# Performance work log

Hardware: AMD Instinct MI355X
Metric: run time of the kernel (lower is better)

## Reference

```python
import jax, jax.numpy as jnp
import numpy as np

B, CIN, H, W = 2, 55, 768, 768
NR, NC = 24, 24      # number of grid-cell rows / cols
CTOP = 36            # block_conv1x1_output[block_num-1] for block_num=2


def _dil_conv_relu(x, w, b, dil):
    # Conv2d(k=5, dilation=dil, padding=2*dil) -> same spatial size, then ReLU
    pad = 2 * dil
    y = jax.lax.conv_general_dilated(
        x, w, window_strides=(1, 1), padding=[(pad, pad), (pad, pad)],
        rhs_dilation=(dil, dil), dimension_numbers=('NCHW', 'OIHW', 'NCHW'))
    return jax.nn.relu(y + b[None, :, None, None])


def setup_inputs() -> dict:
    key = jax.random.key(0)
    ks = jax.random.split(key, 12)
    def p(k, shape, fan_in):
        bound = 1.0 / np.sqrt(fan_in)
        return jax.random.uniform(k, shape, jnp.float32, -bound, bound)
    return {
        'x': jax.random.normal(ks[0], (B, CIN, H, W), dtype=jnp.float32),
        'row_ids': jnp.sort(jax.random.randint(ks[1], (H,), 0, NR)).astype(jnp.int32),
        'col_ids': jnp.sort(jax.random.randint(ks[2], (W,), 0, NC)).astype(jnp.int32),
        'num_row_segs': NR,
        'num_col_segs': NC,
        'w1': p(ks[3], (6, CIN, 5, 5), CIN * 25), 'b1': p(ks[4], (6,), CIN * 25),
        'w2': p(ks[5], (6, CIN, 5, 5), CIN * 25), 'b2': p(ks[6], (6,), CIN * 25),
        'w3': p(ks[7], (6, CIN, 5, 5), CIN * 25), 'b3': p(ks[8], (6,), CIN * 25),
        'w_top': p(ks[9], (CTOP, 18), 18), 'b_top': p(ks[9], (CTOP,), 18),
        'w_bot': p(ks[10], (1, 18), 18), 'b_bot': p(ks[11], (1,), 18),
    }


def reference(x, row_ids, col_ids, num_row_segs, num_col_segs,
              w1, b1, w2, b2, w3, b3, w_top, b_top, w_bot, b_bot):
    b = x.shape[0]
    # --- three dilated conv branches, concat on channels ---
    x1 = _dil_conv_relu(x, w1, b1, 1)
    x2 = _dil_conv_relu(x, w2, b2, 2)
    x3 = _dil_conv_relu(x, w3, b3, 3)
    out_feature = jnp.concatenate((x1, x2, x3), axis=1)  # [B,18,H,W]

    # 1x1 convs as channel matmuls
    top = jnp.einsum('oi,bihw->bohw', w_top, out_feature) + b_top[None, :, None, None]
    bot = jnp.einsum('oi,bihw->bohw', w_bot, out_feature) + b_bot[None, :, None, None]

    # segment one-hot selectors: R [NR,H], C [NC,W]
    R = (row_ids[None, :] == jnp.arange(num_row_segs, dtype=row_ids.dtype)[:, None]).astype(x.dtype)
    C = (col_ids[None, :] == jnp.arange(num_col_segs, dtype=col_ids.dtype)[:, None]).astype(x.dtype)
    cnt = jnp.maximum(R.sum(1)[:, None] * C.sum(1)[None, :], 1.0)  # [NR,NC] cell sizes

    # --- top branch: per-(batch,channel) grid-cell mean, broadcast back ---
    top_sums = jnp.einsum('rh,bkhw,cw->bkrc', R, top, C)           # [B,CTOP,NR,NC]
    top_means = top_sums / cnt
    top_out = top_means[:, :, row_ids, :][:, :, :, col_ids]        # [B,CTOP,H,W]

    # --- bottom branch: mean of sigmoid over cell AND batch (torch.mean over all dims) ---
    sig = jax.nn.sigmoid(bot)                                      # [B,1,H,W]
    bot_sums = jnp.einsum('rh,bkhw,cw->rc', R, sig, C)             # [NR,NC]
    pools_val = bot_sums / (b * cnt)
    bottom_out = jnp.broadcast_to(pools_val[row_ids, :][:, col_ids][None, None],
                                  (b, 1, top.shape[2], top.shape[3]))
    pools = jnp.broadcast_to(pools_val[None, None], (b, 1, num_row_segs, num_col_segs))

    out_x = jnp.concatenate((top_out, out_feature, bottom_out), axis=1)  # [B,55,H,W]
    return out_x, pools
```

## Files before the change

### kernel.cpp

```cpp
#include <hip/hip_runtime.h>
#include <math.h>

#define HH 768
#define WW 768
#define NPIX (HH*WW)
#define NRR 24
#define NCC 24
#define NCELL (NRR*NCC)
#define CTOPC 36
#define NB 2

typedef _Float16 f16x8 __attribute__((ext_vector_type(8)));
typedef float f32x4 __attribute__((ext_vector_type(4)));

__device__ __forceinline__ size_t xt_off(int b) {
  return b ? (size_t)54 * NPIX : 0;
}

#define OFF_WB     0
#define OFF_ZP     38400
#define OFF_FSUM   38656
#define OFF_BOTP   59392
#define OFF_TMEAN  60544
#define OFF_PVAL   102016
#define OFF_BOUNDS 102592

__global__ void prep_kernel(const float* __restrict__ w1, const float* __restrict__ w2,
                            const float* __restrict__ w3,
                            const int* __restrict__ row_ids, const int* __restrict__ col_ids,
                            unsigned int* __restrict__ wB, unsigned int* __restrict__ zp,
                            int* __restrict__ bounds) {
  int t = blockIdx.x * 256 + threadIdx.x;
  if (t < 150 * 256) {
    int frag = t >> 8, r = t & 255;
    int lane = r >> 2, part = r & 3;
    int chb = frag & 1, q = frag >> 1;
    int d = q / 25, tap = q % 25;
    int ky = tap / 5, kx = tap % 5;
    int oc = lane & 15;
    int kk = (lane >> 4) * 8 + part * 2;
    int ch0 = chb * 32 + kk, ch1 = ch0 + 1;
    const float* ws_ = (d == 0) ? w1 : ((d == 1) ? w2 : w3);
    float f0 = (oc < 6 && ch0 < 55) ? ws_[((oc * 55 + ch0) * 5 + ky) * 5 + kx] : 0.f;
    float f1 = (oc < 6 && ch1 < 55) ? ws_[((oc * 55 + ch1) * 5 + ky) * 5 + kx] : 0.f;
    _Float16 g0 = (_Float16)f0, g1 = (_Float16)f1;
    wB[t] = (unsigned int)__builtin_bit_cast(unsigned short, g0) |
            ((unsigned int)__builtin_bit_cast(unsigned short, g1) << 16);
  }
  if (blockIdx.x == 1 && threadIdx.x < 256) zp[threadIdx.x] = 0u;
  if (blockIdx.x == 0 && threadIdx.x < 48) {
    int tt = threadIdx.x;
    const int* ids = (tt < 24) ? row_ids : col_ids;
    int r = tt % 24;
    int s = HH, e = HH;
    for (int h = 0; h < HH; ++h) {
      int v = ids[h];
      if (v >= r && h < s) s = h;
      if (v >= r + 1 && h < e) e = h;
    }
    int base = (tt < 24) ? 0 : 48;
    bounds[base + r] = s;
    bounds[base + 24 + r] = e;
  }
}

__global__ __launch_bounds__(256) void xpose_kernel(const float* __restrict__ x,
                                                    unsigned int* __restrict__ outU) {
  const int b = blockIdx.y;
  const int px = blockIdx.x * 256 + threadIdx.x;
  const float* xb = x + (size_t)b * 55 * NPIX + px;
  unsigned int buf[32];
  #pragma unroll
  for (int cp = 0; cp < 27; ++cp) {
    float f0 = xb[(size_t)(2 * cp) * NPIX];
    float f1 = xb[(size_t)(2 * cp + 1) * NPIX];
    buf[cp] = __builtin_bit_cast(unsigned int, __builtin_amdgcn_cvt_pkrtz(f0, f1));
  }
  buf[27] = __builtin_bit_cast(unsigned int, __builtin_amdgcn_cvt_pkrtz(xb[(size_t)54 * NPIX], 0.f));
  buf[28] = buf[29] = buf[30] = buf[31] = 0u;
  unsigned int* dst = outU + xt_off(b) + (size_t)px * 32;
  #pragma unroll
  for (int i = 0; i < 8; ++i) ((uint4*)dst)[i] = *(uint4*)&buf[i * 4];
}

__global__ __attribute__((amdgpu_flat_work_group_size(384, 384)))
           __attribute__((amdgpu_waves_per_eu(2, 3)))
void conv_kernel(const unsigned int* __restrict__ outU_c,
                 const unsigned int* __restrict__ wB,
                 const unsigned int* __restrict__ zp,
                 const float* __restrict__ b1, const float* __restrict__ b2,
                 const float* __restrict__ b3, float* __restrict__ out) {
  __shared__ __align__(16) unsigned int tile[17600];
  const int tid = threadIdx.x;
  const int lane = tid & 63, wave = tid >> 6;
  const int d = wave >> 1, hh = wave & 1, dil = d + 1;
  const int b = blockIdx.z;
  const int h0 = blockIdx.y * 8, w0 = blockIdx.x * 32;
  const unsigned int* xTb = outU_c + xt_off(b);
  const int col = lane & 15, kq = lane >> 4;

  f32x4 acc[8];
  #pragma unroll
  for (int u = 0; u < 8; ++u) acc[u] = (f32x4){0.f, 0.f, 0.f, 0.f};

  for (int chb = 0; chb < 2; ++chb) {
    #pragma unroll
    for (int k = 0; k < 10; ++k) {
      int idx = k * 384 + tid;
      if (idx < 3520) {
        int pxl = idx >> 2, part = idx & 3;
        int th = pxl / 44, tw = pxl % 44;
        int gh = h0 - 6 + th, gw = w0 - 6 + tw;
        bool ok = ((unsigned)gh < 768u) & ((unsigned)gw < 768u);
        const unsigned int* src = ok
            ? xTb + ((size_t)(gh * 768 + gw)) * 32 + chb * 16 + part * 4
            : zp + (tid & 63) * 4;
        uint4 v = *(const uint4*)src;
        *(uint4*)&tile[pxl * 20 + part * 4] = v;
      }
    }
    __syncthreads();
    for (int ky = 0; ky < 5; ++ky) {
      #pragma unroll
      for (int kx = 0; kx < 5; ++kx) {
        const int fidx = ((d * 25 + ky * 5 + kx) * 2 + chb) << 8;
        f16x8 bfrag = __builtin_bit_cast(f16x8, *(const uint4*)(wB + fidx + lane * 4));
        const int dy = (ky - 2) * dil, dx = (kx - 2) * dil;
        const int thb = hh * 4 + 6 + dy;
        const int twb = col + 6 + dx;
        #pragma unroll
        for (int u = 0; u < 8; ++u) {
          int hr = u >> 1, pc = u & 1;
          int a_addr = ((thb + hr) * 44 + twb + pc * 16) * 20 + kq * 4;
          f16x8 afrag = __builtin_bit_cast(f16x8, *(const uint4*)&tile[a_addr]);
          acc[u] = __builtin_amdgcn_mfma_f32_16x16x32_f16(afrag, bfrag, acc[u], 0, 0, 0);
        }
      }
    }
    __syncthreads();
  }

  float* ot = (float*)tile;
  if (col < 6) {
    #pragma unroll
    for (int u = 0; u < 8; ++u) {
      int hr = hh * 4 + (u >> 1), pc = u & 1;
      int oc = d * 6 + col;
      #pragma unroll
      for (int reg = 0; reg < 4; ++reg) {
        int px = kq * 4 + reg;
        ot[(oc * 8 + hr) * 32 + pc * 16 + px] = acc[u][reg];
      }
    }
  }
  __syncthreads();
  #pragma unroll
  for (int k = 0; k < 3; ++k) {
    int i = k * 384 + tid;
    int oc = i >> 6, rem = i & 63;
    int hr = rem >> 3, f4 = rem & 7;
    float bias = oc < 6 ? b1[oc] : (oc < 12 ? b2[oc - 6] : b3[oc - 12]);
    float4 v = ((float4*)ot)[i];
    v.x = fmaxf(v.x + bias, 0.f); v.y = fmaxf(v.y + bias, 0.f);
    v.z = fmaxf(v.z + bias, 0.f); v.w = fmaxf(v.w + bias, 0.f);
    *(float4*)(out + ((size_t)(b * 55 + 36 + oc)) * NPIX
               + (size_t)(h0 + hr) * 768 + w0 + f4 * 4) = v;
  }
}

__global__ __launch_bounds__(256) void cellsum_kernel(const float* __restrict__ dout,
    const int* __restrict__ bounds,
    const float* __restrict__ w_bot, const float* __restrict__ b_bot,
    float* __restrict__ feat_sums, float* __restrict__ bot_partial) {
  int blk = blockIdx.x;
  int b = blk / NCELL; int rc = blk % NCELL; int r = rc / NCC, c = rc % NCC;
  int rs = bounds[r], re = bounds[24 + r], cs = bounds[48 + c], ce = bounds[72 + c];
  int cw = ce - cs;
  int npix = (re - rs) * cw;
  float facc[18];
  #pragma unroll
  for (int k = 0; k < 18; ++k) facc[k] = 0.f;
  float sacc = 0.f;
  float wb[18];
  #pragma unroll
  for (int k = 0; k < 18; ++k) wb[k] = w_bot[k];
  float bb = b_bot[0];
  const float* fb = dout + ((size_t)b * 55 + 36) * NPIX;
  for (int i = threadIdx.x; i < npix; i += 256) {
    int hh = rs + i / cw, ww = cs + i % cw;
    int pix = hh * WW + ww;
    float dot = bb;
    #pragma unroll
    for (int k = 0; k < 18; ++k) {
      float v = fb[(size_t)k * NPIX + pix];
      facc[k] += v;
      dot += wb[k] * v;
    }
    sacc += 1.f / (1.f + expf(-dot));
  }
  #pragma unroll
  for (int k = 0; k < 18; ++k) {
    #pragma unroll
    for (int off = 32; off; off >>= 1) facc[k] += __shfl_xor(facc[k], off);
  }
  #pragma unroll
  for (int off = 32; off; off >>= 1) sacc += __shfl_xor(sacc, off);
  __shared__ float red[4][19];
  int wv = threadIdx.x >> 6, ln = threadIdx.x & 63;
  if (ln == 0) {
    #pragma unroll
    for (int k = 0; k < 18; ++k) red[wv][k] = facc[k];
    red[wv][18] = sacc;
  }
  __syncthreads();
  if (threadIdx.x < 19) {
    float s = red[0][threadIdx.x] + red[1][threadIdx.x] + red[2][threadIdx.x] + red[3][threadIdx.x];
    if (threadIdx.x < 18) feat_sums[(size_t)blk * 18 + threadIdx.x] = s;
    else bot_partial[blk] = s;
  }
}

__global__ void cellmean_kernel(const float* __restrict__ feat_sums,
    const float* __restrict__ bot_partial, const int* __restrict__ bounds,
    const float* __restrict__ w_top, const float* __restrict__ b_top,
    float* __restrict__ top_means, float* __restrict__ pools_val, float* __restrict__ dout) {
  int t = blockIdx.x * 256 + threadIdx.x;
  if (t < NB * CTOPC * NCELL) {
    int c = t % NCC, r = (t / NCC) % NRR, k = (t / NCELL) % CTOPC, b = t / (NCELL * CTOPC);
    int cnt = (bounds[24 + r] - bounds[r]) * (bounds[72 + c] - bounds[48 + c]);
    float v = 0.f;
    if (cnt > 0) {
      const float* fs = feat_sums + ((size_t)(b * NCELL + r * NCC + c)) * 18;
      float dot = 0.f;
      #pragma unroll
      for (int i = 0; i < 18; ++i) dot += w_top[k * 18 + i] * fs[i];
      v = dot / (float)cnt + b_top[k];
    }
    top_means[t] = v;
  }
  int t2 = t - NB * CTOPC * NCELL;
  if (t2 >= 0 && t2 < NCELL) {
    int r = t2 / NCC, c = t2 % NCC;
    int cnt = (bounds[24 + r] - bounds[r]) * (bounds[72 + c] - bounds[48 + c]);
    if (cnt < 1) cnt = 1;
    float v = (bot_partial[t2] + bot_partial[NCELL + t2]) / (2.f * (float)cnt);
    pools_val[t2] = v;
    dout[(size_t)NB * 55 * NPIX + t2] = v;
    dout[(size_t)NB * 55 * NPIX + NCELL + t2] = v;
  }
}

__global__ __launch_bounds__(256) void bcast_kernel(const float* __restrict__ top_means,
    const float* __restrict__ pools_val, const int* __restrict__ row_ids,
    const int* __restrict__ col_ids, float* __restrict__ out) {
  int w = blockIdx.x * 256 + threadIdx.x;
  int h = blockIdx.y;
  int b = blockIdx.z;
  int r = row_ids[h], c = col_ids[w];
  int pix = h * 768 + w;
  float* ob = out + (size_t)b * 55 * NPIX + pix;
  const float* tm = top_means + (size_t)b * CTOPC * NCELL + r * NCC + c;
  #pragma unroll
  for (int k = 0; k < 36; ++k) ob[(size_t)k * NPIX] = tm[(size_t)k * NCELL];
  ob[(size_t)54 * NPIX] = pools_val[r * NCC + c];
}

extern "C" void kernel_launch(void* const* d_in, const int* in_sizes, int n_in,
                              void* d_out, int out_size, void* d_ws, size_t ws_size,
                              hipStream_t stream) {
  const float* x      = (const float*)d_in[0];
  const int* row_ids  = (const int*)d_in[1];
  const int* col_ids  = (const int*)d_in[2];
  const float* w1     = (const float*)d_in[5];
  const float* b1     = (const float*)d_in[6];
  const float* w2     = (const float*)d_in[7];
  const float* b2     = (const float*)d_in[8];
  const float* w3     = (const float*)d_in[9];
  const float* b3     = (const float*)d_in[10];
  const float* w_top  = (const float*)d_in[11];
  const float* b_top  = (const float*)d_in[12];
  const float* w_bot  = (const float*)d_in[13];
  const float* b_bot  = (const float*)d_in[14];
  float* out = (float*)d_out;
  float* ws  = (float*)d_ws;

  unsigned int* wB   = (unsigned int*)ws + OFF_WB;
  unsigned int* zp   = (unsigned int*)ws + OFF_ZP;
  float* feat_sums   = ws + OFF_FSUM;
  float* bot_partial = ws + OFF_BOTP;
  float* top_means   = ws + OFF_TMEAN;
  float* pools_val   = ws + OFF_PVAL;
  int*   bounds      = (int*)ws + OFF_BOUNDS;
  unsigned int* outU = (unsigned int*)d_out;

  hipLaunchKernelGGL(prep_kernel, dim3(150), dim3(256), 0, stream,
                     w1, w2, w3, row_ids, col_ids, wB, zp, bounds);
  hipLaunchKernelGGL(xpose_kernel, dim3(2304, 2), dim3(256), 0, stream,
                     x, outU);
  hipLaunchKernelGGL(conv_kernel, dim3(24, 96, 2), dim3(384), 0, stream,
                     outU, wB, zp, b1, b2, b3, out);
  hipLaunchKernelGGL(cellsum_kernel, dim3(NB * NCELL), dim3(256), 0, stream,
                     out, bounds, w_bot, b_bot, feat_sums, bot_partial);
  hipLaunchKernelGGL(cellmean_kernel, dim3(165), dim3(256), 0, stream,
                     feat_sums, bot_partial, bounds, w_top, b_top, top_means, pools_val, out);
  hipLaunchKernelGGL(bcast_kernel, dim3(3, 768, 2), dim3(256), 0, stream,
                     top_means, pools_val, row_ids, col_ids, out);
}
```

Measured before the change: 455.3 us.

## Double-buffer conv tile via direct global-to-LDS loads with swizzled layout

The conv kernel tile shrinks from 32 to 16 output columns so two channel-half tiles fit in LDS at once. The second half is staged with global_load_lds while the first half is computed, removing one barrier-separated load phase. LDS slots are XOR-swizzled to avoid bank conflicts, weight fragments are prefetched one tap ahead, and MFMA sections are given raised priority. The halo overhead per output pixel grows with the narrower tile, and the grid is doubled.

```diff
diff --git a/kernel.cpp b/kernel.cpp
--- a/kernel.cpp
+++ b/kernel.cpp
@@ -84,87 +84,107 @@
 }
 
 __global__ __attribute__((amdgpu_flat_work_group_size(384, 384)))
-           __attribute__((amdgpu_waves_per_eu(2, 3)))
+           __attribute__((amdgpu_waves_per_eu(2, 4)))
 void conv_kernel(const unsigned int* __restrict__ outU_c,
                  const unsigned int* __restrict__ wB,
                  const unsigned int* __restrict__ zp,
                  const float* __restrict__ b1, const float* __restrict__ b2,
                  const float* __restrict__ b3, float* __restrict__ out) {
-  __shared__ __align__(16) unsigned int tile[17600];
+  __shared__ __align__(16) unsigned int tile[2][8960];
   const int tid = threadIdx.x;
   const int lane = tid & 63, wave = tid >> 6;
   const int d = wave >> 1, hh = wave & 1, dil = d + 1;
   const int b = blockIdx.z;
-  const int h0 = blockIdx.y * 8, w0 = blockIdx.x * 32;
+  const int h0 = blockIdx.y * 8, w0 = blockIdx.x * 16;
   const unsigned int* xTb = outU_c + xt_off(b);
   const int col = lane & 15, kq = lane >> 4;
 
-  f32x4 acc[8];
-  #pragma unroll
-  for (int u = 0; u < 8; ++u) acc[u] = (f32x4){0.f, 0.f, 0.f, 0.f};
-
-  for (int chb = 0; chb < 2; ++chb) {
-    #pragma unroll
-    for (int k = 0; k < 10; ++k) {
+  auto STAGE = [&](int bufi, int chb) {
+    #pragma unroll
+    for (int k = 0; k < 6; ++k) {
       int idx = k * 384 + tid;
-      if (idx < 3520) {
-        int pxl = idx >> 2, part = idx & 3;
-        int th = pxl / 44, tw = pxl % 44;
+      if (idx < 2240) {
+        int pxl = idx >> 2, slot = idx & 3;
+        int q = slot ^ ((pxl >> 1) & 3);
+        int th = pxl / 28, tw = pxl % 28;
         int gh = h0 - 6 + th, gw = w0 - 6 + tw;
         bool ok = ((unsigned)gh < 768u) & ((unsigned)gw < 768u);
         const unsigned int* src = ok
-            ? xTb + ((size_t)(gh * 768 + gw)) * 32 + chb * 16 + part * 4
-            : zp + (tid & 63) * 4;
-        uint4 v = *(const uint4*)src;
-        *(uint4*)&tile[pxl * 20 + part * 4] = v;
+            ? xTb + ((size_t)(gh * 768 + gw)) * 32 + chb * 16 + q * 4
+            : zp + (lane) * 4;
+        unsigned int* dst = &tile[bufi][(k * 384 + (tid & ~63)) * 4];
+        __builtin_amdgcn_global_load_lds(
+            (const __attribute__((address_space(1))) void*)src,
+            (__attribute__((address_space(3))) void*)dst, 16, 0, 0);
       }
     }
-    __syncthreads();
-    for (int ky = 0; ky < 5; ++ky) {
+  };
+
+  f32x4 acc[4];
+  #pragma unroll
+  for (int u = 0; u < 4; ++u) acc[u] = (f32x4){0.f, 0.f, 0.f, 0.f};
+
+  auto COMPUTE = [&](int bufi, int chb) {
+    const unsigned int* tb = &tile[bufi][0];
+    const unsigned int* wBc = wB + d * 12800 + chb * 256;
+    uint4 bf = *(const uint4*)(wBc + lane * 4);
+    #pragma unroll
+    for (int tap = 0; tap < 25; ++tap) {
+      uint4 bfn = bf;
+      if (tap < 24) bfn = *(const uint4*)(wBc + (size_t)(tap + 1) * 512 + lane * 4);
+      const int ky = tap / 5, kx = tap % 5;
+      const int dy = (ky - 2) * dil, dx = (kx - 2) * dil;
+      const int thb = hh * 4 + 6 + dy;
+      const int twb = col + 6 + dx;
+      f16x8 bfrag = __builtin_bit_cast(f16x8, bf);
+      __builtin_amdgcn_s_setprio(1);
       #pragma unroll
-      for (int kx = 0; kx < 5; ++kx) {
-        const int fidx = ((d * 25 + ky * 5 + kx) * 2 + chb) << 8;
-        f16x8 bfrag = __builtin_bit_cast(f16x8, *(const uint4*)(wB + fidx + lane * 4));
-        const int dy = (ky - 2) * dil, dx = (kx - 2) * dil;
-        const int thb = hh * 4 + 6 + dy;
-        const int twb = col + 6 + dx;
-        #pragma unroll
-        for (int u = 0; u < 8; ++u) {
-          int hr = u >> 1, pc = u & 1;
-          int a_addr = ((thb + hr) * 44 + twb + pc * 16) * 20 + kq * 4;
-          f16x8 afrag = __builtin_bit_cast(f16x8, *(const uint4*)&tile[a_addr]);
-          acc[u] = __builtin_amdgcn_mfma_f32_16x16x32_f16(afrag, bfrag, acc[u], 0, 0, 0);
-        }
+      for (int u = 0; u < 4; ++u) {
+        int pxl = (thb + u) * 28 + twb;
+        int slot = kq ^ ((pxl >> 1) & 3);
+        f16x8 afrag = __builtin_bit_cast(f16x8, *(const uint4*)&tb[pxl * 16 + slot * 4]);
+        acc[u] = __builtin_amdgcn_mfma_f32_16x16x32_f16(afrag, bfrag, acc[u], 0, 0, 0);
       }
-    }
-    __syncthreads();
-  }
-
-  float* ot = (float*)tile;
+      __builtin_amdgcn_s_setprio(0);
+      bf = bfn;
+    }
+  };
+
+  STAGE(0, 0);
+  __syncthreads();
+  STAGE(1, 1);
+  COMPUTE(0, 0);
+  __syncthreads();
+  COMPUTE(1, 1);
+  __syncthreads();
+
+  float* ot = (float*)&tile[0][0];
   if (col < 6) {
     #pragma unroll
-    for (int u = 0; u < 8; ++u) {
-      int hr = hh * 4 + (u >> 1), pc = u & 1;
+    for (int u = 0; u < 4; ++u) {
+      int row = hh * 4 + u;
       int oc = d * 6 + col;
       #pragma unroll
       for (int reg = 0; reg < 4; ++reg) {
         int px = kq * 4 + reg;
-        ot[(oc * 8 + hr) * 32 + pc * 16 + px] = acc[u][reg];
+        ot[(oc * 8 + row) * 16 + px] = acc[u][reg];
       }
     }
   }
   __syncthreads();
   #pragma unroll
-  for (int k = 0; k < 3; ++k) {
+  for (int k = 0; k < 2; ++k) {
     int i = k * 384 + tid;
-    int oc = i >> 6, rem = i & 63;
-    int hr = rem >> 3, f4 = rem & 7;
-    float bias = oc < 6 ? b1[oc] : (oc < 12 ? b2[oc - 6] : b3[oc - 12]);
-    float4 v = ((float4*)ot)[i];
-    v.x = fmaxf(v.x + bias, 0.f); v.y = fmaxf(v.y + bias, 0.f);
-    v.z = fmaxf(v.z + bias, 0.f); v.w = fmaxf(v.w + bias, 0.f);
-    *(float4*)(out + ((size_t)(b * 55 + 36 + oc)) * NPIX
-               + (size_t)(h0 + hr) * 768 + w0 + f4 * 4) = v;
+    if (i < 576) {
+      int oc = i >> 5, rem = i & 31;
+      int row = rem >> 2, f4 = rem & 3;
+      float bias = oc < 6 ? b1[oc] : (oc < 12 ? b2[oc - 6] : b3[oc - 12]);
+      float4 v = ((float4*)ot)[i];
+      v.x = fmaxf(v.x + bias, 0.f); v.y = fmaxf(v.y + bias, 0.f);
+      v.z = fmaxf(v.z + bias, 0.f); v.w = fmaxf(v.w + bias, 0.f);
+      *(float4*)(out + ((size_t)(b * 55 + 36 + oc)) * NPIX
+                 + (size_t)(h0 + row) * 768 + w0 + f4 * 4) = v;
+    }
   }
 }
 
@@ -297,7 +317,7 @@
                      w1, w2, w3, row_ids, col_ids, wB, zp, bounds);
   hipLaunchKernelGGL(xpose_kernel, dim3(2304, 2), dim3(256), 0, stream,
                      x, outU);
-  hipLaunchKernelGGL(conv_kernel, dim3(24, 96, 2), dim3(384), 0, stream,
+  hipLaunchKernelGGL(conv_kernel, dim3(48, 96, 2), dim3(384), 0, stream,
                      outU, wB, zp, b1, b2, b3, out);
   hipLaunchKernelGGL(cellsum_kernel, dim3(NB * NCELL), dim3(256), 0, stream,
                      out, bounds, w_bot, b_bot, feat_sums, bot_partial);
```

Result: slower. 469.4 us (+3.1%).
